# Performance work log

Measured on AMD Instinct MI355X. Metric: run time of the kernel, lower is better.

## Reference

```python
import jax, jax.numpy as jnp
import numpy as np

B, H, W_IMG, K, OUT = 65536, 28, 28, 3, 10
OH = H - K + 1  # 26

def setup_inputs() -> dict:
    key = jax.random.key(0)
    k1, k2, k3 = jax.random.split(key, 3)
    x = jax.random.normal(k1, (B, H * W_IMG), dtype=jnp.float32)
    conv_w = jax.random.normal(k2, (K, K), dtype=jnp.float32)
    Wlin = jax.random.normal(k3, (OH * OH, OUT), dtype=jnp.float32)
    b = jnp.zeros((1, OUT), dtype=jnp.float32)
    return {"x": x, "conv_w": conv_w, "W": Wlin, "b": b}

def reference(x, conv_w, W, b):
    imgs = x.reshape(-1, 1, H, W_IMG)  # [B,1,28,28] NCHW
    kern = conv_w.reshape(1, 1, K, K)  # OIHW
    conv = jax.lax.conv_general_dilated(
        imgs, kern, window_strides=(1, 1), padding='VALID',
        dimension_numbers=('NCHW', 'OIHW', 'NCHW'))  # [B,1,26,26]
    feat = jax.nn.relu(conv.reshape(conv.shape[0], -1))  # [B,676]
    return feat @ W + b  # [B,10]
```

## Files before the change

### kernel.cpp

```cpp
#include <hip/hip_runtime.h>
#include <cstdint>

#define IMG_ELEMS 784
#define NIMG_GRP 16
#define IMG_STRIDE_DW 788
#define STAGE_DW (NIMG_GRP * IMG_STRIDE_DW)
#define SCRATCH_DW 2048
#define BLOCKS 512

typedef __attribute__((ext_vector_type(8))) short short8;
typedef __attribute__((ext_vector_type(4))) float f32x4;

union ABu { uint32_t u[4]; short8 v; };

typedef const __attribute__((address_space(1))) void* gp1_t;
typedef __attribute__((address_space(3))) void* lp3_t;

__device__ inline uint32_t pk_bf16(float a, float b) {
    uint32_t r;
    asm("v_cvt_pk_bf16_f32 %0, %1, %2" : "=v"(r) : "v"(a), "v"(b));
    return r;
}

__device__ inline void stage_group(const float* __restrict__ x, float* stage,
                                   int grp, int widb, int lane) {
    const float* gsrc = x + (size_t)grp * (NIMG_GRP * IMG_ELEMS);
#pragma unroll
    for (int k = 0; k < 4; ++k) {
        const int im = widb * 4 + k;
        const float* s = gsrc + im * IMG_ELEMS;
        float* dbase = stage + im * IMG_STRIDE_DW;
#pragma unroll
        for (int j = 0; j < 3; ++j) {
            __builtin_amdgcn_global_load_lds((gp1_t)(s + j * 256 + lane * 4),
                                             (lp3_t)(dbase + j * 256), 16, 0, 0);
        }
        if (lane < 4) {
            __builtin_amdgcn_global_load_lds((gp1_t)(s + 768 + lane * 4),
                                             (lp3_t)(dbase + 768), 16, 0, 0);
        }
    }
}

__global__ __launch_bounds__(256, 2) void fused_digit_dma_kernel(
    const float* __restrict__ x,
    const float* __restrict__ cw9,
    const float* __restrict__ Wlin,
    const float* __restrict__ bias,
    float* __restrict__ out,
    int ngroups, int grp_per_blk)
{
    __shared__ float smem[STAGE_DW + SCRATCH_DW];
    float* stagebuf = smem;

    const int tid  = threadIdx.x;
    const int lane = tid & 63;
    const int widb = tid >> 6;
    const int rc = lane & 15;
    const int g  = lane >> 4;

    float cw[9];
#pragma unroll
    for (int k = 0; k < 9; ++k) cw[k] = cw9[k];
    const float bv = (rc < 10) ? bias[rc] : 0.0f;

    const int R0 = (widb < 2) ? widb * 7 : 14 + (widb - 2) * 6;
    const int RC = (widb < 2) ? 7 : 6;

    ABu bf[7];
#pragma unroll
    for (int rr = 0; rr < 7; ++rr) {
        const int r = R0 + rr;
#pragma unroll
        for (int m = 0; m < 4; ++m) {
            const int c0 = 8 * g + 2 * m;
            const int c1 = c0 + 1;
            const bool v0 = (rr < RC) && (c0 < 26) && (rc < 10);
            const bool v1 = (rr < RC) && (c1 < 26) && (rc < 10);
            const float w0 = v0 ? Wlin[(r * 26 + c0) * 10 + rc] : 0.0f;
            const float w1 = v1 ? Wlin[(r * 26 + c1) * 10 + rc] : 0.0f;
            bf[rr].u[m] = pk_bf16(w0, w1);
        }
    }

    const int co0 = 8 * g;
    const int co1 = (8 * g + 4 > 24) ? 24 : 8 * g + 4;
    const int co2 = (8 * g + 8 > 24) ? 24 : 8 * g + 8;

    const int gstart = blockIdx.x * grp_per_blk;

    if (gstart < ngroups) stage_group(x, stagebuf, gstart, widb, lane);

    for (int i = 0; i < grp_per_blk; ++i) {
        const int grp = gstart + i;
        if (grp >= ngroups) break;

        asm volatile("s_waitcnt vmcnt(0)" ::: "memory");
        __syncthreads();

        const float* ib = &stagebuf[rc * IMG_STRIDE_DW];
        float accr[3][8];
#pragma unroll
        for (int s = 0; s < 3; ++s)
#pragma unroll
            for (int j = 0; j < 8; ++j) accr[s][j] = 0.0f;
        f32x4 acc = {0.f, 0.f, 0.f, 0.f};

#pragma unroll
        for (int t = 0; t < 9; ++t) {
            if (t < RC + 2) {
                const float* rp = ib + (R0 + t) * 28;
                float in[12];
                *(float4*)&in[0] = *(const float4*)(rp + co0);
                *(float4*)&in[4] = *(const float4*)(rp + co1);
                *(float4*)&in[8] = *(const float4*)(rp + co2);

                const int s0 = t % 3;
                const int s1 = (t + 2) % 3;
                const int s2 = (t + 1) % 3;

                if (t < RC) {
#pragma unroll
                    for (int j = 0; j < 8; ++j)
                        accr[s0][j] = fmaf(in[j], cw[0],
                                      fmaf(in[j + 1], cw[1],
                                      fmaf(in[j + 2], cw[2], accr[s0][j])));
                }
                if (t >= 1 && t <= RC) {
#pragma unroll
                    for (int j = 0; j < 8; ++j)
                        accr[s1][j] = fmaf(in[j], cw[3],
                                      fmaf(in[j + 1], cw[4],
                                      fmaf(in[j + 2], cw[5], accr[s1][j])));
                }
                if (t >= 2) {
#pragma unroll
                    for (int j = 0; j < 8; ++j)
                        accr[s2][j] = fmaf(in[j], cw[6],
                                      fmaf(in[j + 1], cw[7],
                                      fmaf(in[j + 2], cw[8], accr[s2][j])));
                    ABu a;
#pragma unroll
                    for (int m = 0; m < 4; ++m)
                        a.u[m] = pk_bf16(fmaxf(accr[s2][2 * m], 0.f),
                                         fmaxf(accr[s2][2 * m + 1], 0.f));
                    acc = __builtin_amdgcn_mfma_f32_16x16x32_bf16(
                              a.v, bf[t - 2].v, acc, 0, 0, 0);
#pragma unroll
                    for (int j = 0; j < 8; ++j) accr[s2][j] = 0.0f;
                }
            }
        }

        float* sc = &smem[STAGE_DW + (i & 1) * 1024];
        *reinterpret_cast<f32x4*>(sc + widb * 256 + lane * 4) = acc;
        __syncthreads();

        if (i + 1 < grp_per_blk && grp + 1 < ngroups)
            stage_group(x, stagebuf, grp + 1, widb, lane);

        if (widb == 0) {
            const float* scr = sc + lane * 4;
            f32x4 s0 = *reinterpret_cast<const f32x4*>(scr);
            f32x4 s1 = *reinterpret_cast<const f32x4*>(scr + 256);
            f32x4 s2 = *reinterpret_cast<const f32x4*>(scr + 512);
            f32x4 s3 = *reinterpret_cast<const f32x4*>(scr + 768);
            if (rc < 10) {
                float* po = out + ((size_t)grp * NIMG_GRP + (size_t)g * 4) * 10 + rc;
#pragma unroll
                for (int q = 0; q < 4; ++q)
                    po[q * 10] = s0[q] + s1[q] + s2[q] + s3[q] + bv;
            }
        }
    }
}

extern "C" void kernel_launch(void* const* d_in, const int* in_sizes, int n_in,
                              void* d_out, int out_size, void* d_ws, size_t ws_size,
                              hipStream_t stream) {
    const float* x   = (const float*)d_in[0];
    const float* cw  = (const float*)d_in[1];
    const float* W   = (const float*)d_in[2];
    const float* b   = (const float*)d_in[3];
    float* out = (float*)d_out;

    const int nimg    = in_sizes[0] / IMG_ELEMS;
    const int ngroups = nimg / NIMG_GRP;
    const int gpb     = (ngroups + BLOCKS - 1) / BLOCKS;

    hipLaunchKernelGGL(fused_digit_dma_kernel, dim3(BLOCKS), dim3(256), 0, stream,
                       x, cw, W, b, out, ngroups, gpb);
}
```

Baseline: 45.80 us.

## Double-buffer image staging with 8-wave blocks splitting conv rows

Each block now has 8 waves and two LDS staging buffers. The next 16-image group is DMA'd into the alternate buffer before the current group is computed, with a partial vmcnt wait so only the current group's loads must have landed. The 26 output rows are split across 8 waves instead of 4, which shrinks per-wave B-fragment registers and the unrolled loop. The grid drops to 256 blocks with one resident block per CU, because LDS use roughly doubles. The final cross-wave reduction now sums 8 partials instead of 4.

```diff
diff --git a/kernel.cpp b/kernel.cpp
--- a/kernel.cpp
+++ b/kernel.cpp
@@ -5,8 +5,9 @@
 #define NIMG_GRP 16
 #define IMG_STRIDE_DW 788
 #define STAGE_DW (NIMG_GRP * IMG_STRIDE_DW)
-#define SCRATCH_DW 2048
-#define BLOCKS 512
+#define NWAVES 8
+#define SCRATCH_DW (NWAVES * 256)
+#define BLOCKS 256
 
 typedef __attribute__((ext_vector_type(8))) short short8;
 typedef __attribute__((ext_vector_type(4))) float f32x4;
@@ -22,36 +23,36 @@
     return r;
 }
 
-__device__ inline void stage_group(const float* __restrict__ x, float* stage,
+__device__ inline void stage_group(const float* __restrict__ x, float* dst,
                                    int grp, int widb, int lane) {
     const float* gsrc = x + (size_t)grp * (NIMG_GRP * IMG_ELEMS);
 #pragma unroll
-    for (int k = 0; k < 4; ++k) {
-        const int im = widb * 4 + k;
+    for (int k = 0; k < 2; ++k) {
+        const int im = widb * 2 + k;
         const float* s = gsrc + im * IMG_ELEMS;
-        float* dbase = stage + im * IMG_STRIDE_DW;
-#pragma unroll
-        for (int j = 0; j < 3; ++j) {
+        float* d = dst + im * IMG_STRIDE_DW;
+#pragma unroll
+        for (int j = 0; j < 3; ++j)
             __builtin_amdgcn_global_load_lds((gp1_t)(s + j * 256 + lane * 4),
-                                             (lp3_t)(dbase + j * 256), 16, 0, 0);
-        }
-        if (lane < 4) {
+                                             (lp3_t)(d + j * 256), 16, 0, 0);
+        if (lane < 4)
             __builtin_amdgcn_global_load_lds((gp1_t)(s + 768 + lane * 4),
-                                             (lp3_t)(dbase + 768), 16, 0, 0);
-        }
+                                             (lp3_t)(d + 768), 16, 0, 0);
     }
 }
 
-__global__ __launch_bounds__(256, 2) void fused_digit_dma_kernel(
+__global__ __launch_bounds__(512, 1) void fused_digit_dbuf_kernel(
     const float* __restrict__ x,
     const float* __restrict__ cw9,
     const float* __restrict__ Wlin,
     const float* __restrict__ bias,
     float* __restrict__ out,
-    int ngroups, int grp_per_blk)
+    int ngroups, int gpb)
 {
-    __shared__ float smem[STAGE_DW + SCRATCH_DW];
-    float* stagebuf = smem;
+    __shared__ float smem[2 * STAGE_DW + SCRATCH_DW];
+    float* const buf0 = smem;
+    float* const buf1 = smem + STAGE_DW;
+    float* const scr  = smem + 2 * STAGE_DW;
 
     const int tid  = threadIdx.x;
     const int lane = tid & 63;
@@ -64,12 +65,12 @@
     for (int k = 0; k < 9; ++k) cw[k] = cw9[k];
     const float bv = (rc < 10) ? bias[rc] : 0.0f;
 
-    const int R0 = (widb < 2) ? widb * 7 : 14 + (widb - 2) * 6;
-    const int RC = (widb < 2) ? 7 : 6;
-
-    ABu bf[7];
-#pragma unroll
-    for (int rr = 0; rr < 7; ++rr) {
+    const int R0 = (widb < 2) ? 4 * widb : 8 + 3 * (widb - 2);
+    const int RC = (widb < 2) ? 4 : 3;
+
+    ABu bf[4];
+#pragma unroll
+    for (int rr = 0; rr < 4; ++rr) {
         const int r = R0 + rr;
 #pragma unroll
         for (int m = 0; m < 4; ++m) {
@@ -87,18 +88,26 @@
     const int co1 = (8 * g + 4 > 24) ? 24 : 8 * g + 4;
     const int co2 = (8 * g + 8 > 24) ? 24 : 8 * g + 8;
 
-    const int gstart = blockIdx.x * grp_per_blk;
-
-    if (gstart < ngroups) stage_group(x, stagebuf, gstart, widb, lane);
-
-    for (int i = 0; i < grp_per_blk; ++i) {
+    const int gstart = blockIdx.x * gpb;
+
+    if (gstart < ngroups) stage_group(x, buf0, gstart, widb, lane);
+
+    for (int i = 0; i < gpb; ++i) {
         const int grp = gstart + i;
         if (grp >= ngroups) break;
 
-        asm volatile("s_waitcnt vmcnt(0)" ::: "memory");
+        float* const cur = (i & 1) ? buf1 : buf0;
+        float* const alt = (i & 1) ? buf0 : buf1;
+
+        if (i + 1 < gpb && grp + 1 < ngroups) {
+            stage_group(x, alt, grp + 1, widb, lane);
+            asm volatile("s_waitcnt vmcnt(8)" ::: "memory");
+        } else {
+            asm volatile("s_waitcnt vmcnt(0)" ::: "memory");
+        }
         __syncthreads();
 
-        const float* ib = &stagebuf[rc * IMG_STRIDE_DW];
+        const float* ib = cur + rc * IMG_STRIDE_DW;
         float accr[3][8];
 #pragma unroll
         for (int s = 0; s < 3; ++s)
@@ -107,7 +116,7 @@
         f32x4 acc = {0.f, 0.f, 0.f, 0.f};
 
 #pragma unroll
-        for (int t = 0; t < 9; ++t) {
+        for (int t = 0; t < 6; ++t) {
             if (t < RC + 2) {
                 const float* rp = ib + (R0 + t) * 28;
                 float in[12];
@@ -152,24 +161,22 @@
             }
         }
 
-        float* sc = &smem[STAGE_DW + (i & 1) * 1024];
-        *reinterpret_cast<f32x4*>(sc + widb * 256 + lane * 4) = acc;
+        *reinterpret_cast<f32x4*>(scr + widb * 256 + lane * 4) = acc;
         __syncthreads();
 
-        if (i + 1 < grp_per_blk && grp + 1 < ngroups)
-            stage_group(x, stagebuf, grp + 1, widb, lane);
-
         if (widb == 0) {
-            const float* scr = sc + lane * 4;
-            f32x4 s0 = *reinterpret_cast<const f32x4*>(scr);
-            f32x4 s1 = *reinterpret_cast<const f32x4*>(scr + 256);
-            f32x4 s2 = *reinterpret_cast<const f32x4*>(scr + 512);
-            f32x4 s3 = *reinterpret_cast<const f32x4*>(scr + 768);
+            const float* sp = scr + lane * 4;
+            float s[4] = {0.f, 0.f, 0.f, 0.f};
+#pragma unroll
+            for (int w = 0; w < NWAVES; ++w) {
+                f32x4 p = *reinterpret_cast<const f32x4*>(sp + w * 256);
+#pragma unroll
+                for (int q = 0; q < 4; ++q) s[q] += p[q];
+            }
             if (rc < 10) {
                 float* po = out + ((size_t)grp * NIMG_GRP + (size_t)g * 4) * 10 + rc;
 #pragma unroll
-                for (int q = 0; q < 4; ++q)
-                    po[q * 10] = s0[q] + s1[q] + s2[q] + s3[q] + bv;
+                for (int q = 0; q < 4; ++q) po[q * 10] = s[q] + bv;
             }
         }
     }
@@ -188,6 +195,6 @@
     const int ngroups = nimg / NIMG_GRP;
     const int gpb     = (ngroups + BLOCKS - 1) / BLOCKS;
 
-    hipLaunchKernelGGL(fused_digit_dma_kernel, dim3(BLOCKS), dim3(256), 0, stream,
+    hipLaunchKernelGGL(fused_digit_dbuf_kernel, dim3(BLOCKS), dim3(512), 0, stream,
                        x, cw, W, b, out, ngroups, gpb);
 }
```

New measurement: 51.63 us. 12.7% more time.

## Shrink LDS scratch to fit three blocks per CU with grid-stride loop

Applied to the files above, without the earlier changes.

Drops the double-buffered reduction scratch to a single buffer, which cuts per-block LDS enough for three 256-thread blocks to share a CU. Launch bounds and grid size are raised to match, and the contiguous per-block group range becomes a grid-stride loop. The wave that does the final cross-wave sum and output store now rotates with the group index, spreading that tail work across waves. The aim is more loads in flight to hide global-memory latency on a bandwidth-bound kernel. The cost is tighter register budgets and reuse of one scratch buffer, which relies on the existing barriers for ordering.

```diff
diff --git a/kernel.cpp b/kernel.cpp
--- a/kernel.cpp
+++ b/kernel.cpp
@@ -5,8 +5,9 @@
 #define NIMG_GRP 16
 #define IMG_STRIDE_DW 788
 #define STAGE_DW (NIMG_GRP * IMG_STRIDE_DW)
-#define SCRATCH_DW 2048
-#define BLOCKS 512
+#define NWAVES 4
+#define SCRATCH_DW (NWAVES * 256)
+#define BLOCKS 768
 
 typedef __attribute__((ext_vector_type(8))) short short8;
 typedef __attribute__((ext_vector_type(4))) float f32x4;
@@ -31,27 +32,26 @@
         const float* s = gsrc + im * IMG_ELEMS;
         float* dbase = stage + im * IMG_STRIDE_DW;
 #pragma unroll
-        for (int j = 0; j < 3; ++j) {
+        for (int j = 0; j < 3; ++j)
             __builtin_amdgcn_global_load_lds((gp1_t)(s + j * 256 + lane * 4),
                                              (lp3_t)(dbase + j * 256), 16, 0, 0);
-        }
-        if (lane < 4) {
+        if (lane < 4)
             __builtin_amdgcn_global_load_lds((gp1_t)(s + 768 + lane * 4),
                                              (lp3_t)(dbase + 768), 16, 0, 0);
-        }
     }
 }
 
-__global__ __launch_bounds__(256, 2) void fused_digit_dma_kernel(
+__global__ __launch_bounds__(256, 3) void fused_digit_dma3_kernel(
     const float* __restrict__ x,
     const float* __restrict__ cw9,
     const float* __restrict__ Wlin,
     const float* __restrict__ bias,
     float* __restrict__ out,
-    int ngroups, int grp_per_blk)
+    int ngroups)
 {
     __shared__ float smem[STAGE_DW + SCRATCH_DW];
-    float* stagebuf = smem;
+    float* const stagebuf = smem;
+    float* const scr      = smem + STAGE_DW;
 
     const int tid  = threadIdx.x;
     const int lane = tid & 63;
@@ -87,18 +87,15 @@
     const int co1 = (8 * g + 4 > 24) ? 24 : 8 * g + 4;
     const int co2 = (8 * g + 8 > 24) ? 24 : 8 * g + 8;
 
-    const int gstart = blockIdx.x * grp_per_blk;
+    if (blockIdx.x < (unsigned)ngroups)
+        stage_group(x, stagebuf, blockIdx.x, widb, lane);
 
-    if (gstart < ngroups) stage_group(x, stagebuf, gstart, widb, lane);
-
-    for (int i = 0; i < grp_per_blk; ++i) {
-        const int grp = gstart + i;
-        if (grp >= ngroups) break;
+    for (int grp = blockIdx.x; grp < ngroups; grp += gridDim.x) {
 
         asm volatile("s_waitcnt vmcnt(0)" ::: "memory");
         __syncthreads();
 
-        const float* ib = &stagebuf[rc * IMG_STRIDE_DW];
+        const float* ib = stagebuf + rc * IMG_STRIDE_DW;
         float accr[3][8];
 #pragma unroll
         for (int s = 0; s < 3; ++s)
@@ -152,24 +149,23 @@
             }
         }
 
-        float* sc = &smem[STAGE_DW + (i & 1) * 1024];
-        *reinterpret_cast<f32x4*>(sc + widb * 256 + lane * 4) = acc;
+        *reinterpret_cast<f32x4*>(scr + widb * 256 + lane * 4) = acc;
         __syncthreads();
 
-        if (i + 1 < grp_per_blk && grp + 1 < ngroups)
-            stage_group(x, stagebuf, grp + 1, widb, lane);
+        const int nxt = grp + gridDim.x;
+        if (nxt < ngroups) stage_group(x, stagebuf, nxt, widb, lane);
 
-        if (widb == 0) {
-            const float* scr = sc + lane * 4;
-            f32x4 s0 = *reinterpret_cast<const f32x4*>(scr);
-            f32x4 s1 = *reinterpret_cast<const f32x4*>(scr + 256);
-            f32x4 s2 = *reinterpret_cast<const f32x4*>(scr + 512);
-            f32x4 s3 = *reinterpret_cast<const f32x4*>(scr + 768);
+        if (widb == (grp & 3)) {
+            const float* sp = scr + lane * 4;
+            f32x4 p0 = *reinterpret_cast<const f32x4*>(sp);
+            f32x4 p1 = *reinterpret_cast<const f32x4*>(sp + 256);
+            f32x4 p2 = *reinterpret_cast<const f32x4*>(sp + 512);
+            f32x4 p3 = *reinterpret_cast<const f32x4*>(sp + 768);
             if (rc < 10) {
                 float* po = out + ((size_t)grp * NIMG_GRP + (size_t)g * 4) * 10 + rc;
 #pragma unroll
                 for (int q = 0; q < 4; ++q)
-                    po[q * 10] = s0[q] + s1[q] + s2[q] + s3[q] + bv;
+                    po[q * 10] = p0[q] + p1[q] + p2[q] + p3[q] + bv;
             }
         }
     }
@@ -186,8 +182,7 @@
 
     const int nimg    = in_sizes[0] / IMG_ELEMS;
     const int ngroups = nimg / NIMG_GRP;
-    const int gpb     = (ngroups + BLOCKS - 1) / BLOCKS;
 
-    hipLaunchKernelGGL(fused_digit_dma_kernel, dim3(BLOCKS), dim3(256), 0, stream,
-                       x, cw, W, b, out, ngroups, gpb);
+    hipLaunchKernelGGL(fused_digit_dma3_kernel, dim3(BLOCKS), dim3(256), 0, stream,
+                       x, cw, W, b, out, ngroups);
 }
```

New measurement: 56.81 us. 24.1% more time.
